# Optimization experiments

Hardware: AMD Instinct MI355X
Metric: run time of the kernel (lower is better)

The kernel has to match this reference:

```python
import jax, jax.numpy as jnp
import numpy as np

N, E, F, C, H, L, ED = 100000, 1600000, 128, 16, 2, 2, 4
EPS = 1e-5
NEG_SLOPE = 0.2


def setup_inputs() -> dict:
    key = jax.random.key(0)
    ks = jax.random.split(key, 32)
    s = 0.1
    inp = {
        "x": jax.random.normal(ks[0], (N, F), dtype=jnp.float32),
        "edge_index": jax.random.randint(ks[1], (2, E), 0, N, dtype=jnp.int64),
        "edge_attr": jax.random.uniform(ks[2], (E, ED), dtype=jnp.float32),
        "embed_W": jax.random.normal(ks[3], (F, C)) * s,
        "embed_b": jnp.zeros((C,), jnp.float32),
        "ln0_w": jnp.ones((C,), jnp.float32),
        "ln0_b": jnp.zeros((C,), jnp.float32),
        "Wl": jax.random.normal(ks[4], (L, C, H * C)) * s,
        "bl": jnp.zeros((L, H * C), jnp.float32),
        "Wr": jax.random.normal(ks[5], (L, C, H * C)) * s,
        "br": jnp.zeros((L, H * C), jnp.float32),
        "We": jax.random.normal(ks[6], (L, ED, H * C)) * s,
        "att": jax.random.normal(ks[7], (L, H, C)) * s,
        "gat_b": jnp.zeros((L, H * C), jnp.float32),
        "n1_w": jnp.ones((L, H * C), jnp.float32),
        "n1_b": jnp.zeros((L, H * C), jnp.float32),
        "lin_W": jax.random.normal(ks[8], (L, H * C, C)) * s,
        "lin_b": jnp.zeros((L, C), jnp.float32),
        "n2_w": jnp.ones((L, C), jnp.float32),
        "n2_b": jnp.zeros((L, C), jnp.float32),
    }
    return inp


def _node_ln(v, w, b):
    # torch.nn.LayerNorm over the feature dim (per node)
    mu = v.mean(-1, keepdims=True)
    var = ((v - mu) ** 2).mean(-1, keepdims=True)
    return (v - mu) / jnp.sqrt(var + EPS) * w + b


def _graph_ln(v, w, b):
    # PyG norm.LayerNorm(mode='graph'): normalize over ALL nodes and channels
    mu = v.mean()
    vc = v - mu
    return vc / jnp.sqrt((vc * vc).mean() + EPS) * w + b


def reference(x, edge_index, edge_attr, embed_W, embed_b, ln0_w, ln0_b,
              Wl, bl, Wr, br, We, att, gat_b, n1_w, n1_b,
              lin_W, lin_b, n2_w, n2_b):
    n = x.shape[0]
    heads, c = att.shape[1], att.shape[2]
    layers = Wl.shape[0]

    # node embedding MLP (dropout = identity in eval)
    h = jax.nn.relu(_node_ln(x @ embed_W + embed_b, ln0_w, ln0_b))

    # add self-loops (fill_value=0.0 -> zero edge features, lin_edge has no bias)
    loop = jnp.arange(n)
    src = jnp.concatenate([edge_index[0], loop])
    dst = jnp.concatenate([edge_index[1], loop])

    hs = [h]
    for i in range(layers):
        xl = (h @ Wl[i] + bl[i]).reshape(n, heads, c)   # source transform (x_j)
        xr = (h @ Wr[i] + br[i]).reshape(n, heads, c)   # target transform (x_i)
        ew = (edge_attr @ We[i]).reshape(-1, heads, c)
        ew = jnp.concatenate([ew, jnp.zeros((n, heads, c), ew.dtype)], axis=0)

        msg = xl[src] + xr[dst] + ew                      # [E+N, H, C]
        logits = jnp.einsum('ehc,hc->eh', jax.nn.leaky_relu(msg, NEG_SLOPE), att[i])
        m = jax.ops.segment_max(logits, dst, num_segments=n)
        ex = jnp.exp(logits - m[dst])
        den = jax.ops.segment_sum(ex, dst, num_segments=n)
        alpha = ex / den[dst]                             # segment softmax over dst

        g = jax.ops.segment_sum(alpha[..., None] * xl[src], dst, num_segments=n)
        g = g.reshape(n, heads * c) + gat_b[i]

        g = jax.nn.relu(_graph_ln(g, n1_w[i], n1_b[i]))
        g = g @ lin_W[i] + lin_b[i]
        g = _graph_ln(g, n2_w[i], n2_b[i])
        h = jax.nn.relu(g + h)                            # residual + relu
        hs.append(h)

    # JumpingKnowledge mode='max': elementwise max over layer outputs
    return jnp.max(jnp.stack(hs, axis=0), axis=0)
```

## Files before the change

### kernel.cpp

```cpp
#include <hip/hip_runtime.h>

#define N_NODES 100000
#define N_EDGES 1600000
#define NF 128
#define NC 16
#define NH 2
#define HC 32
#define NL 2
#define NED 4
#define EPS 1e-5f
#define NEG 0.2f
#define NBUCK 196
#define P1_CHUNK 4096
#define P1_BLKS ((N_EDGES + P1_CHUNK - 1) / P1_CHUNK)
#define AGG_BLKS ((N_NODES + 7) / 8)
#define MID_BLKS ((N_NODES + 15) / 16)

__device__ __forceinline__ unsigned short f2bf(float f) {
    unsigned int u = __float_as_uint(f);
    u += 0x7fffu + ((u >> 16) & 1u);
    return (unsigned short)(u >> 16);
}
__device__ __forceinline__ float bf2f(unsigned short u) {
    return __uint_as_float(((unsigned int)u) << 16);
}
__device__ __forceinline__ unsigned int pack_bf2(float a, float b) {
    return (unsigned int)f2bf(a) | ((unsigned int)f2bf(b) << 16);
}
__device__ __forceinline__ float bflo(int u) {
    return __uint_as_float(((unsigned int)u) << 16);
}
__device__ __forceinline__ float bfhi(int u) {
    return __uint_as_float(((unsigned int)u) & 0xffff0000u);
}

__global__ __launch_bounds__(256) void k_embed(
    const float* __restrict__ x, const float* __restrict__ W,
    const float* __restrict__ b, const float* __restrict__ lnw,
    const float* __restrict__ lnb, float* __restrict__ h, float* __restrict__ jk)
{
    __shared__ float Ws[NF * NC];
    __shared__ float xs[16][NF + 4];
    const int t = threadIdx.x;
    for (int i = t; i < NF * NC; i += 256) Ws[i] = W[i];
    const int n0 = blockIdx.x * 16;
    for (int i = t; i < 16 * NF; i += 256) {
        int r = i >> 7, f = i & (NF - 1);
        int n = n0 + r;
        xs[r][f] = (n < N_NODES) ? x[(size_t)n * NF + f] : 0.f;
    }
    __syncthreads();
    const int r = t >> 4;
    const int c = t & 15;
    const int n = n0 + r;
    float acc = b[c];
#pragma unroll 16
    for (int f = 0; f < NF; ++f) acc += xs[r][f] * Ws[f * NC + c];
    float s = acc;
    for (int m = 8; m >= 1; m >>= 1) s += __shfl_xor(s, m, 16);
    float mu = s * (1.f / 16.f);
    float d = acc - mu;
    float v = d * d;
    for (int m = 8; m >= 1; m >>= 1) v += __shfl_xor(v, m, 16);
    float inv = rsqrtf(v * (1.f / 16.f) + EPS);
    float out = fmaxf(d * inv * lnw[c] + lnb[c], 0.f);
    if (n < N_NODES) {
        h[(size_t)n * NC + c]  = out;
        jk[(size_t)n * NC + c] = out;
    }
}

__global__ __launch_bounds__(256) void k_bhist(
    const int* __restrict__ dst, int* __restrict__ bcnt)
{
    __shared__ int hist[256];
    const int t = threadIdx.x;
    hist[t] = 0;
    __syncthreads();
    const int e0 = blockIdx.x * P1_CHUNK;
    const int cnt = min(P1_CHUNK, N_EDGES - e0);
    for (int i = t; i < cnt; i += 256)
        atomicAdd(&hist[dst[e0 + i] >> 9], 1);
    __syncthreads();
    if (hist[t] > 0) atomicAdd(&bcnt[t], hist[t]);
}

__global__ __launch_bounds__(256) void k_bscan(
    const int* __restrict__ bcnt, int* __restrict__ bbase, int* __restrict__ bcur)
{
    __shared__ int tmp[256];
    const int t = threadIdx.x;
    int v0 = bcnt[t];
    tmp[t] = v0;
    __syncthreads();
    for (int off = 1; off < 256; off <<= 1) {
        int v = (t >= off) ? tmp[t - off] : 0;
        __syncthreads();
        tmp[t] += v;
        __syncthreads();
    }
    int excl = tmp[t] - v0;
    bbase[t] = excl;
    bcur[t]  = excl;
    if (t == 255) bbase[256] = tmp[t];
}

__global__ __launch_bounds__(256) void k_pass1(
    const int* __restrict__ src, const int* __restrict__ dst,
    const float4* __restrict__ ea4, int* __restrict__ bcur,
    int4* __restrict__ tmp_rec)
{
    __shared__ int2 stage[P1_CHUNK];
    __shared__ unsigned char bstage[P1_CHUNK];
    __shared__ int hist[256];
    __shared__ int exc[256];
    __shared__ int gbase[256];
    __shared__ int scanbuf[256];
    const int t = threadIdx.x;
    const int e0 = blockIdx.x * P1_CHUNK;
    const int cnt = min(P1_CHUNK, N_EDGES - e0);
    hist[t] = 0;
    __syncthreads();
    int mys[16], myb[16], myp[16];
    int nv = 0;
#pragma unroll
    for (int k = 0; k < 16; ++k) {
        int i = k * 256 + t;
        if (i < cnt) {
            int e = e0 + i;
            int d = dst[e];
            mys[nv] = src[e];
            myb[nv] = d >> 9;
            myp[nv] = (e << 9) | (d & 511);
            atomicAdd(&hist[d >> 9], 1);
            ++nv;
        }
    }
    __syncthreads();
    int hv = hist[t];
    scanbuf[t] = hv;
    __syncthreads();
    for (int off = 1; off < 256; off <<= 1) {
        int v = (t >= off) ? scanbuf[t - off] : 0;
        __syncthreads();
        scanbuf[t] += v;
        __syncthreads();
    }
    int ex = scanbuf[t] - hv;
    hist[t] = ex;
    exc[t]  = ex;
    __syncthreads();
    for (int k = 0; k < nv; ++k) {
        int pos = atomicAdd(&hist[myb[k]], 1);
        stage[pos]  = make_int2(mys[k], myp[k]);
        bstage[pos] = (unsigned char)myb[k];
    }
    __syncthreads();
    {
        int c = hist[t] - exc[t];
        gbase[t] = (c > 0) ? atomicAdd(&bcur[t], c) : 0;
    }
    __syncthreads();
    for (int i = t; i < cnt; i += 256) {
        int b = bstage[i];
        int2 se = stage[i];
        int e  = (int)(((unsigned int)se.y) >> 9);
        int dl = se.y & 511;
        float4 ea = ea4[e];
        int gpos = gbase[b] + (i - exc[b]);
        tmp_rec[gpos] = make_int4(se.x, dl,
                                  (int)pack_bf2(ea.x, ea.y),
                                  (int)pack_bf2(ea.z, ea.w));
    }
}

__global__ __launch_bounds__(256) void k_pass2(
    const int* __restrict__ bbase, const int4* __restrict__ tmp_rec,
    int* __restrict__ offsets, int4* __restrict__ csr)
{
    __shared__ int hist[512];
    __shared__ int cur[512];
    __shared__ int scanbuf[256];
    const int b = blockIdx.x, t = threadIdx.x;
    const int ebeg = bbase[b], eend = bbase[b + 1];
    hist[t] = 0; hist[t + 256] = 0;
    __syncthreads();
    for (int i = ebeg + t; i < eend; i += 256)
        atomicAdd(&hist[tmp_rec[i].y], 1);
    __syncthreads();
    int a0 = hist[2 * t], a1 = hist[2 * t + 1];
    int pair = a0 + a1;
    scanbuf[t] = pair;
    __syncthreads();
    for (int off = 1; off < 256; off <<= 1) {
        int v = (t >= off) ? scanbuf[t - off] : 0;
        __syncthreads();
        scanbuf[t] += v;
        __syncthreads();
    }
    int ex2 = scanbuf[t] - pair;
    cur[2 * t]     = ex2;
    cur[2 * t + 1] = ex2 + a0;
    __syncthreads();
    const int n0 = b * 512;
#pragma unroll
    for (int k = 0; k < 2; ++k) {
        int i = t + k * 256;
        int n = n0 + i;
        if (n < N_NODES) offsets[n] = ebeg + cur[i];
    }
    if (b == NBUCK - 1 && t == 0) offsets[N_NODES] = N_EDGES;
    __syncthreads();
    for (int i = ebeg + t; i < eend; i += 256) {
        int4 rec = tmp_rec[i];
        int pos = ebeg + atomicAdd(&cur[rec.y], 1);
        csr[pos] = rec;
    }
}

__global__ __launch_bounds__(256) void k_trans(
    const float* __restrict__ h, const float* __restrict__ Wl, const float* __restrict__ bl,
    const float* __restrict__ Wr, const float* __restrict__ br,
    unsigned short* __restrict__ xl, unsigned short* __restrict__ xr)
{
    __shared__ float Wls[NC * HC], Wrs[NC * HC];
    __shared__ float hs[8][NC + 1];
    const int t = threadIdx.x;
    for (int i = t; i < NC * HC; i += 256) { Wls[i] = Wl[i]; Wrs[i] = Wr[i]; }
    const int n0 = blockIdx.x * 8;
    for (int i = t; i < 8 * NC; i += 256) {
        int r = i >> 4, c = i & 15;
        int n = n0 + r;
        hs[r][c] = (n < N_NODES) ? h[(size_t)n * NC + c] : 0.f;
    }
    __syncthreads();
    const int r = t >> 5;
    const int j = t & 31;
    const int n = n0 + r;
    float al = bl[j], ar = br[j];
#pragma unroll
    for (int c = 0; c < NC; ++c) {
        float hv = hs[r][c];
        al += hv * Wls[c * HC + j];
        ar += hv * Wrs[c * HC + j];
    }
    if (n < N_NODES) {
        xl[(size_t)n * HC + j] = f2bf(al);
        xr[(size_t)n * HC + j] = f2bf(ar);
    }
}

__device__ __forceinline__ float head_sum(float p) {
    p += __shfl_xor(p, 1, 16);
    p += __shfl_xor(p, 2, 16);
    p += __shfl_xor(p, 4, 16);
    p += __shfl_xor(p, 8, 16);
    return p;
}

__global__ __launch_bounds__(256) void k_agg(
    const int* __restrict__ offsets, const int4* __restrict__ csr,
    const float* __restrict__ We, const float* __restrict__ att,
    const float* __restrict__ gat_b,
    const unsigned short* __restrict__ xl, const unsigned short* __restrict__ xr,
    float* __restrict__ g, float2* __restrict__ part)
{
    __shared__ float Wes[NED * HC];
    __shared__ float atts[HC], gbs[HC];
    const int t = threadIdx.x;
    if (t < NED * HC) Wes[t] = We[t];
    if (t < HC) { atts[t] = att[t]; gbs[t] = gat_b[t]; }
    __syncthreads();
    const int grp = t >> 5;
    const int j   = t & 31;
    const int d = blockIdx.x * 8 + grp;
    float gv = 0.f;
    if (d < N_NODES) {
        const float aj = atts[j];
        const float w0 = Wes[j], w1 = Wes[HC + j], w2 = Wes[2 * HC + j], w3 = Wes[3 * HC + j];
        const float xld = bf2f(xl[(size_t)d * HC + j]);
        const float xrd = bf2f(xr[(size_t)d * HC + j]);
        float m = xld + xrd;
        m = (m > 0.f) ? m : NEG * m;
        float eh = __expf(head_sum(m * aj));
        float acc = eh * xld;
        float den = eh;
        const int base = offsets[d];
        const int deg  = offsets[d + 1] - base;
        int k = 0;
        for (; k + 4 <= deg; k += 4) {
            const int b0 = base + k;
            const int4 r0 = csr[b0],     r1 = csr[b0 + 1];
            const int4 r2 = csr[b0 + 2], r3 = csr[b0 + 3];
            const float x0 = bf2f(xl[(size_t)r0.x * HC + j]);
            const float x1 = bf2f(xl[(size_t)r1.x * HC + j]);
            const float x2 = bf2f(xl[(size_t)r2.x * HC + j]);
            const float x3 = bf2f(xl[(size_t)r3.x * HC + j]);
            float m0 = x0 + xrd + bflo(r0.z) * w0 + bfhi(r0.z) * w1 + bflo(r0.w) * w2 + bfhi(r0.w) * w3;
            float m1 = x1 + xrd + bflo(r1.z) * w0 + bfhi(r1.z) * w1 + bflo(r1.w) * w2 + bfhi(r1.w) * w3;
            float m2 = x2 + xrd + bflo(r2.z) * w0 + bfhi(r2.z) * w1 + bflo(r2.w) * w2 + bfhi(r2.w) * w3;
            float m3 = x3 + xrd + bflo(r3.z) * w0 + bfhi(r3.z) * w1 + bflo(r3.w) * w2 + bfhi(r3.w) * w3;
            m0 = (m0 > 0.f) ? m0 : NEG * m0;
            m1 = (m1 > 0.f) ? m1 : NEG * m1;
            m2 = (m2 > 0.f) ? m2 : NEG * m2;
            m3 = (m3 > 0.f) ? m3 : NEG * m3;
            float p0 = m0 * aj, p1 = m1 * aj, p2 = m2 * aj, p3 = m3 * aj;
            p0 += __shfl_xor(p0, 1, 16); p1 += __shfl_xor(p1, 1, 16);
            p2 += __shfl_xor(p2, 1, 16); p3 += __shfl_xor(p3, 1, 16);
            p0 += __shfl_xor(p0, 2, 16); p1 += __shfl_xor(p1, 2, 16);
            p2 += __shfl_xor(p2, 2, 16); p3 += __shfl_xor(p3, 2, 16);
            p0 += __shfl_xor(p0, 4, 16); p1 += __shfl_xor(p1, 4, 16);
            p2 += __shfl_xor(p2, 4, 16); p3 += __shfl_xor(p3, 4, 16);
            p0 += __shfl_xor(p0, 8, 16); p1 += __shfl_xor(p1, 8, 16);
            p2 += __shfl_xor(p2, 8, 16); p3 += __shfl_xor(p3, 8, 16);
            const float ee0 = __expf(p0), ee1 = __expf(p1);
            const float ee2 = __expf(p2), ee3 = __expf(p3);
            acc += ee0 * x0 + ee1 * x1 + ee2 * x2 + ee3 * x3;
            den += ee0 + ee1 + ee2 + ee3;
        }
        for (; k < deg; ++k) {
            const int4 r = csr[base + k];
            const float xv = bf2f(xl[(size_t)r.x * HC + j]);
            float mm = xv + xrd + bflo(r.z) * w0 + bfhi(r.z) * w1 + bflo(r.w) * w2 + bfhi(r.w) * w3;
            mm = (mm > 0.f) ? mm : NEG * mm;
            const float ee = __expf(head_sum(mm * aj));
            acc += ee * xv;
            den += ee;
        }
        gv = acc / den + gbs[j];
        g[(size_t)d * HC + j] = gv;
    }
    float s = gv, ss = gv * gv;
    for (int m = 32; m >= 1; m >>= 1) { s += __shfl_xor(s, m); ss += __shfl_xor(ss, m); }
    __shared__ float sr[4], ssr[4];
    const int w = t >> 6;
    if ((t & 63) == 0) { sr[w] = s; ssr[w] = ss; }
    __syncthreads();
    if (t == 0) part[blockIdx.x] = make_float2(sr[0] + sr[1] + sr[2] + sr[3],
                                               ssr[0] + ssr[1] + ssr[2] + ssr[3]);
}

__global__ __launch_bounds__(256) void k_red(
    const float2* __restrict__ part, int n, double* __restrict__ out)
{
    const int t = threadIdx.x;
    double s = 0.0, ss = 0.0;
    for (int i = t; i < n; i += 256) {
        float2 p = part[i];
        s += (double)p.x; ss += (double)p.y;
    }
    for (int m = 32; m >= 1; m >>= 1) { s += __shfl_xor(s, m); ss += __shfl_xor(ss, m); }
    __shared__ double sr[4], ssr[4];
    const int w = t >> 6;
    if ((t & 63) == 0) { sr[w] = s; ssr[w] = ss; }
    __syncthreads();
    if (t == 0) {
        out[0] = sr[0] + sr[1] + sr[2] + sr[3];
        out[1] = ssr[0] + ssr[1] + ssr[2] + ssr[3];
    }
}

__global__ __launch_bounds__(256) void k_mid(
    const float* __restrict__ g,
    const float* __restrict__ n1w, const float* __restrict__ n1b,
    const float* __restrict__ linW, const float* __restrict__ linb,
    const double* __restrict__ stats1, float* __restrict__ g2,
    float2* __restrict__ part)
{
    __shared__ float Ws[HC * NC];
    __shared__ float rs[16][HC + 1];
    const int t = threadIdx.x;
    for (int i = t; i < HC * NC; i += 256) Ws[i] = linW[i];
    const double cnt = (double)N_NODES * HC;
    const double mud = stats1[0] / cnt;
    const float mu  = (float)mud;
    const float var = (float)(stats1[1] / cnt - mud * mud);
    const float inv = rsqrtf(var + EPS);
    const int n0 = blockIdx.x * 16;
    for (int i = t; i < 16 * HC; i += 256) {
        int r = i >> 5, j = i & 31;
        int n = n0 + r;
        float v = (n < N_NODES) ? g[(size_t)n * HC + j] : mu;
        v = (v - mu) * inv * n1w[j] + n1b[j];
        rs[r][j] = fmaxf(v, 0.f);
    }
    __syncthreads();
    const int r = t >> 4, c = t & 15;
    const int n = n0 + r;
    float acc = linb[c];
#pragma unroll
    for (int j = 0; j < HC; ++j) acc += rs[r][j] * Ws[j * NC + c];
    float val = (n < N_NODES) ? acc : 0.f;
    if (n < N_NODES) g2[(size_t)n * NC + c] = acc;
    float s = val, ss = val * val;
    for (int m = 32; m >= 1; m >>= 1) { s += __shfl_xor(s, m); ss += __shfl_xor(ss, m); }
    __shared__ float sr[4], ssr[4];
    const int w = t >> 6;
    if ((t & 63) == 0) { sr[w] = s; ssr[w] = ss; }
    __syncthreads();
    if (t == 0) part[blockIdx.x] = make_float2(sr[0] + sr[1] + sr[2] + sr[3],
                                               ssr[0] + ssr[1] + ssr[2] + ssr[3]);
}

__global__ __launch_bounds__(256) void k_ftrans(
    const float* __restrict__ g2, const float* __restrict__ n2w,
    const float* __restrict__ n2b, const double* __restrict__ stats2,
    float* __restrict__ h, float* __restrict__ jk,
    const float* __restrict__ Wl, const float* __restrict__ bl,
    const float* __restrict__ Wr, const float* __restrict__ br,
    unsigned short* __restrict__ xl, unsigned short* __restrict__ xr)
{
    __shared__ float Wls[NC * HC], Wrs[NC * HC];
    __shared__ float hs[8][NC + 1];
    const int t = threadIdx.x;
    for (int i = t; i < NC * HC; i += 256) { Wls[i] = Wl[i]; Wrs[i] = Wr[i]; }
    const double cnt = (double)N_NODES * NC;
    const double mud = stats2[0] / cnt;
    const float mu  = (float)mud;
    const float var = (float)(stats2[1] / cnt - mud * mud);
    const float inv = rsqrtf(var + EPS);
    const int n0 = blockIdx.x * 8;
    if (t < 8 * NC) {
        int r = t >> 4, c = t & 15;
        int n = n0 + r;
        if (n < N_NODES) {
            size_t idx = (size_t)n * NC + c;
            float v = (g2[idx] - mu) * inv * n2w[c] + n2b[c];
            float hn = fmaxf(v + h[idx], 0.f);
            h[idx] = hn;
            jk[idx] = fmaxf(jk[idx], hn);
            hs[r][c] = hn;
        } else hs[r][c] = 0.f;
    }
    __syncthreads();
    const int r = t >> 5;
    const int j = t & 31;
    const int n = n0 + r;
    float al = bl[j], ar = br[j];
#pragma unroll
    for (int c = 0; c < NC; ++c) {
        float hv = hs[r][c];
        al += hv * Wls[c * HC + j];
        ar += hv * Wrs[c * HC + j];
    }
    if (n < N_NODES) {
        xl[(size_t)n * HC + j] = f2bf(al);
        xr[(size_t)n * HC + j] = f2bf(ar);
    }
}

__global__ __launch_bounds__(256) void k_final(
    const float* __restrict__ g2, const float* __restrict__ n2w,
    const float* __restrict__ n2b, const double* __restrict__ stats2,
    float* __restrict__ h, float* __restrict__ jk)
{
    const int i = blockIdx.x * 256 + threadIdx.x;
    if (i >= N_NODES * NC) return;
    const double cnt = (double)N_NODES * NC;
    const double mud = stats2[0] / cnt;
    const float mu  = (float)mud;
    const float var = (float)(stats2[1] / cnt - mud * mud);
    const float inv = rsqrtf(var + EPS);
    const int c = i & (NC - 1);
    float v = (g2[i] - mu) * inv * n2w[c] + n2b[c];
    float hn = fmaxf(v + h[i], 0.f);
    h[i] = hn;
    jk[i] = fmaxf(jk[i], hn);
}

extern "C" void kernel_launch(void* const* d_in, const int* in_sizes, int n_in,
                              void* d_out, int out_size, void* d_ws, size_t ws_size,
                              hipStream_t stream)
{
    const float* x     = (const float*)d_in[0];
    const int*   eidx  = (const int*)d_in[1];
    const float* eattr = (const float*)d_in[2];
    const float* embW  = (const float*)d_in[3];
    const float* embB  = (const float*)d_in[4];
    const float* ln0w  = (const float*)d_in[5];
    const float* ln0b  = (const float*)d_in[6];
    const float* Wl    = (const float*)d_in[7];
    const float* bl    = (const float*)d_in[8];
    const float* Wr    = (const float*)d_in[9];
    const float* br    = (const float*)d_in[10];
    const float* We    = (const float*)d_in[11];
    const float* att   = (const float*)d_in[12];
    const float* gatb  = (const float*)d_in[13];
    const float* n1w   = (const float*)d_in[14];
    const float* n1b   = (const float*)d_in[15];
    const float* linW  = (const float*)d_in[16];
    const float* linb  = (const float*)d_in[17];
    const float* n2w   = (const float*)d_in[18];
    const float* n2b   = (const float*)d_in[19];
    float* out = (float*)d_out;

    char* ws = (char*)d_ws;
    double* stats = (double*)ws;
    char* p = ws + 1024;
    int* bcnt = (int*)p; p += 1024;
    int* bbase = (int*)p; p += 4096;
    int* bcur  = (int*)p; p += 1024;
    int* offsets = (int*)p; p += (size_t)(N_NODES + 64) * 4;
    float* g = (float*)p; p += (size_t)N_NODES * HC * 4;
    int4* csr = (int4*)p; p += (size_t)N_EDGES * 16;
    int4* tmp_rec = (int4*)p;
    char* q = p;
    p += (size_t)N_EDGES * 16;
    float* hq = (float*)q; q += (size_t)N_NODES * NC * 4;
    unsigned short* xlq = (unsigned short*)q; q += (size_t)N_NODES * HC * 2;
    unsigned short* xrq = (unsigned short*)q; q += (size_t)N_NODES * HC * 2;
    float* g2q = (float*)q;
    float2* part1 = (float2*)p; p += (size_t)AGG_BLKS * 8;
    float2* part2 = (float2*)p; p += (size_t)MID_BLKS * 8;

    const int* srcp = eidx;
    const int* dstp = eidx + N_EDGES;

    hipMemsetAsync(bcnt, 0, 1024, stream);
    k_bhist<<<P1_BLKS, 256, 0, stream>>>(dstp, bcnt);
    k_bscan<<<1, 256, 0, stream>>>(bcnt, bbase, bcur);
    k_pass1<<<P1_BLKS, 256, 0, stream>>>(srcp, dstp, (const float4*)eattr,
                                         bcur, tmp_rec);
    k_pass2<<<NBUCK, 256, 0, stream>>>(bbase, tmp_rec, offsets, csr);

    k_embed<<<(N_NODES + 15) / 16, 256, 0, stream>>>(x, embW, embB, ln0w, ln0b, hq, out);

    k_trans<<<(N_NODES + 7) / 8, 256, 0, stream>>>(hq, Wl, bl, Wr, br, xlq, xrq);
    k_agg<<<AGG_BLKS, 256, 0, stream>>>(
        offsets, csr, We, att, gatb, xlq, xrq, g, part1);
    k_red<<<1, 256, 0, stream>>>(part1, AGG_BLKS, stats);
    k_mid<<<MID_BLKS, 256, 0, stream>>>(
        g, n1w, n1b, linW, linb, stats, g2q, part2);
    k_red<<<1, 256, 0, stream>>>(part2, MID_BLKS, stats + 2);
    k_ftrans<<<(N_NODES + 7) / 8, 256, 0, stream>>>(
        g2q, n2w, n2b, stats + 2, hq, out,
        Wl + NC * HC, bl + HC, Wr + NC * HC, br + HC, xlq, xrq);
    k_agg<<<AGG_BLKS, 256, 0, stream>>>(
        offsets, csr, We + NED * HC, att + HC, gatb + HC, xlq, xrq, g, part1);
    k_red<<<1, 256, 0, stream>>>(part1, AGG_BLKS, stats);
    k_mid<<<MID_BLKS, 256, 0, stream>>>(
        g, n1w + HC, n1b + HC, linW + HC * NC, linb + NC, stats, g2q, part2);
    k_red<<<1, 256, 0, stream>>>(part2, MID_BLKS, stats + 2);
    k_final<<<(N_NODES * NC + 255) / 256, 256, 0, stream>>>(
        g2q, n2w + NC, n2b + NC, stats + 2, hq, out);
}
```

Before: 493.7 us.

## Vectorize embed loads and use 32-bit offsets in aggregation gathers

The embed kernel now loads x with float4, stores W transposed in shared memory, and runs the dot product on float4 reads to cut LDS instruction count. The aggregation kernel computes gather addresses as 32-bit byte offsets instead of 64-bit size_t index math. It also replaces the leaky-ReLU select with fmaxf. These are micro-optimizations that save ALU and address work, and the 32-bit offsets rely on the xl buffer staying under 4 GB.

```diff
diff --git a/kernel.cpp b/kernel.cpp
--- a/kernel.cpp
+++ b/kernel.cpp
@@ -33,29 +33,42 @@
 __device__ __forceinline__ float bfhi(int u) {
     return __uint_as_float(((unsigned int)u) & 0xffff0000u);
 }
+__device__ __forceinline__ float bf_gather(const unsigned short* base, unsigned boff) {
+    return bf2f(*(const unsigned short*)((const char*)base + boff));
+}
 
 __global__ __launch_bounds__(256) void k_embed(
     const float* __restrict__ x, const float* __restrict__ W,
     const float* __restrict__ b, const float* __restrict__ lnw,
     const float* __restrict__ lnb, float* __restrict__ h, float* __restrict__ jk)
 {
-    __shared__ float Ws[NF * NC];
-    __shared__ float xs[16][NF + 4];
-    const int t = threadIdx.x;
-    for (int i = t; i < NF * NC; i += 256) Ws[i] = W[i];
+    __shared__ __align__(16) float WsT[NC][NF + 4];
+    __shared__ __align__(16) float xs[16][NF + 4];
+    const int t = threadIdx.x;
+    for (int i = t; i < NF * NC; i += 256) {
+        int f = i >> 4, c = i & 15;
+        WsT[c][f] = W[i];
+    }
     const int n0 = blockIdx.x * 16;
-    for (int i = t; i < 16 * NF; i += 256) {
-        int r = i >> 7, f = i & (NF - 1);
+    const float4* x4 = (const float4*)x;
+    for (int i = t; i < 16 * (NF / 4); i += 256) {
+        int r = i >> 5, f4 = i & 31;
         int n = n0 + r;
-        xs[r][f] = (n < N_NODES) ? x[(size_t)n * NF + f] : 0.f;
+        float4 v = (n < N_NODES) ? x4[(size_t)n * (NF / 4) + f4]
+                                 : make_float4(0.f, 0.f, 0.f, 0.f);
+        *(float4*)&xs[r][f4 * 4] = v;
     }
     __syncthreads();
     const int r = t >> 4;
     const int c = t & 15;
     const int n = n0 + r;
     float acc = b[c];
-#pragma unroll 16
-    for (int f = 0; f < NF; ++f) acc += xs[r][f] * Ws[f * NC + c];
+#pragma unroll
+    for (int f4 = 0; f4 < NF / 4; ++f4) {
+        float4 xv = *(const float4*)&xs[r][f4 * 4];
+        float4 wv = *(const float4*)&WsT[c][f4 * 4];
+        acc += xv.x * wv.x + xv.y * wv.y + xv.z * wv.z + xv.w * wv.w;
+    }
     float s = acc;
     for (int m = 8; m >= 1; m >>= 1) s += __shfl_xor(s, m, 16);
     float mu = s * (1.f / 16.f);
@@ -278,10 +291,11 @@
     if (d < N_NODES) {
         const float aj = atts[j];
         const float w0 = Wes[j], w1 = Wes[HC + j], w2 = Wes[2 * HC + j], w3 = Wes[3 * HC + j];
-        const float xld = bf2f(xl[(size_t)d * HC + j]);
-        const float xrd = bf2f(xr[(size_t)d * HC + j]);
+        const unsigned jb = (unsigned)(j << 1);
+        const float xld = bf_gather(xl, ((unsigned)d << 6) + jb);
+        const float xrd = bf_gather(xr, ((unsigned)d << 6) + jb);
         float m = xld + xrd;
-        m = (m > 0.f) ? m : NEG * m;
+        m = fmaxf(m, NEG * m);
         float eh = __expf(head_sum(m * aj));
         float acc = eh * xld;
         float den = eh;
@@ -292,18 +306,18 @@
             const int b0 = base + k;
             const int4 r0 = csr[b0],     r1 = csr[b0 + 1];
             const int4 r2 = csr[b0 + 2], r3 = csr[b0 + 3];
-            const float x0 = bf2f(xl[(size_t)r0.x * HC + j]);
-            const float x1 = bf2f(xl[(size_t)r1.x * HC + j]);
-            const float x2 = bf2f(xl[(size_t)r2.x * HC + j]);
-            const float x3 = bf2f(xl[(size_t)r3.x * HC + j]);
+            const float x0 = bf_gather(xl, ((unsigned)r0.x << 6) + jb);
+            const float x1 = bf_gather(xl, ((unsigned)r1.x << 6) + jb);
+            const float x2 = bf_gather(xl, ((unsigned)r2.x << 6) + jb);
+            const float x3 = bf_gather(xl, ((unsigned)r3.x << 6) + jb);
             float m0 = x0 + xrd + bflo(r0.z) * w0 + bfhi(r0.z) * w1 + bflo(r0.w) * w2 + bfhi(r0.w) * w3;
             float m1 = x1 + xrd + bflo(r1.z) * w0 + bfhi(r1.z) * w1 + bflo(r1.w) * w2 + bfhi(r1.w) * w3;
             float m2 = x2 + xrd + bflo(r2.z) * w0 + bfhi(r2.z) * w1 + bflo(r2.w) * w2 + bfhi(r2.w) * w3;
             float m3 = x3 + xrd + bflo(r3.z) * w0 + bfhi(r3.z) * w1 + bflo(r3.w) * w2 + bfhi(r3.w) * w3;
-            m0 = (m0 > 0.f) ? m0 : NEG * m0;
-            m1 = (m1 > 0.f) ? m1 : NEG * m1;
-            m2 = (m2 > 0.f) ? m2 : NEG * m2;
-            m3 = (m3 > 0.f) ? m3 : NEG * m3;
+            m0 = fmaxf(m0, NEG * m0);
+            m1 = fmaxf(m1, NEG * m1);
+            m2 = fmaxf(m2, NEG * m2);
+            m3 = fmaxf(m3, NEG * m3);
             float p0 = m0 * aj, p1 = m1 * aj, p2 = m2 * aj, p3 = m3 * aj;
             p0 += __shfl_xor(p0, 1, 16); p1 += __shfl_xor(p1, 1, 16);
             p2 += __shfl_xor(p2, 1, 16); p3 += __shfl_xor(p3, 1, 16);
@@ -320,9 +334,9 @@
         }
         for (; k < deg; ++k) {
             const int4 r = csr[base + k];
-            const float xv = bf2f(xl[(size_t)r.x * HC + j]);
+            const float xv = bf_gather(xl, ((unsigned)r.x << 6) + jb);
             float mm = xv + xrd + bflo(r.z) * w0 + bfhi(r.z) * w1 + bflo(r.w) * w2 + bfhi(r.w) * w3;
-            mm = (mm > 0.f) ? mm : NEG * mm;
+            mm = fmaxf(mm, NEG * mm);
             const float ee = __expf(head_sum(mm * aj));
             acc += ee * xv;
             den += ee;
```

New measurement: 478.4 us. -3.1%, faster.
